# Kernel optimization log

Hardware: AMD Instinct MI355X
Metric: run time of the kernel (lower is better)

## Reference

```python
import jax, jax.numpy as jnp
import numpy as np

B, T, I, H, O, R = 128, 1024, 64, 512, 32, 2
TAU = 0.2
NOISE_STD = 0.05


def setup_inputs() -> dict:
    key = jax.random.key(0)
    ks = jax.random.split(key, 12)
    def xavier(k, shape):
        fan_in, fan_out = shape[1], shape[0]
        lim = float(np.sqrt(6.0 / (fan_in + fan_out)))
        return jax.random.uniform(k, shape, jnp.float32, -lim, lim)
    return {
        "u": jax.random.normal(ks[0], (B, T, I), jnp.float32),
        "x0": jax.random.normal(ks[1], (B, H), jnp.float32),
        "noise": jax.random.normal(ks[2], (T, B, H), jnp.float32),
        "Win_w": xavier(ks[3], (H, I)),
        "Win_b": jnp.zeros((H,), jnp.float32),
        "Wout_w": xavier(ks[4], (O, H)),
        "Wout_b": jax.random.normal(ks[5], (O,), jnp.float32) * 0.01,
        "M_rnn": xavier(ks[6], (H, R)),
        "N_rnn": xavier(ks[7], (H, R)),
        "L_tb": xavier(ks[8], (H, R)),
        "M_tb": xavier(ks[9], (H, R)),
        "N_tb": xavier(ks[10], (H, R)),
    }


def reference(u, x0, noise, Win_w, Win_b, Wout_w, Wout_b,
              M_rnn, N_rnn, L_tb, M_tb, N_tb):
    # mode='cont', form='rate', adv=False
    Hdim = x0.shape[1]
    scale_rnn = 1.0 / Hdim
    scale_tb = 1.0 / (Hdim * Hdim)
    # precompute input projection for all timesteps: [T, B, H]
    inp_t = jnp.transpose(jnp.einsum('bti,hi->bth', u, Win_w) + Win_b, (1, 0, 2))

    def step(x, xs):
        ip, nz = xs                                # [B,H] each
        r = jnp.tanh(x)                            # rate form
        rec_rnn = (r @ N_rnn) @ M_rnn.T * scale_rnn
        rec_tb = ((r @ M_tb) * (r @ N_tb)) @ L_tb.T * scale_tb
        rec_x = rec_rnn + rec_tb + ip
        x_new = x + NOISE_STD * nz + TAU * (-x + rec_x)
        return x_new, x_new

    x_final, traj_t = jax.lax.scan(step, x0, (inp_t, noise))
    traj = jnp.transpose(traj_t, (1, 0, 2))        # [B,T,H]
    output = jnp.tanh(traj) @ Wout_w.T + Wout_b    # [B,T,O]
    return output, x_final, traj
```

## Files before the change

kernel.cpp:

```cpp
#include <hip/hip_runtime.h>

constexpr int kB = 128;
constexpr int kT = 1024;
constexpr int kI = 64;
constexpr int kH = 512;
constexpr int kO = 32;
constexpr float kTau = 0.2f;
constexpr float kNoise = 0.05f;

__device__ __forceinline__ float fast_tanh(float x) {
    float e = __expf(2.0f * x);
    return 1.0f - 2.0f * __builtin_amdgcn_rcpf(e + 1.0f);
}

#define BARW() do { asm volatile("s_waitcnt lgkmcnt(0)" ::: "memory"); \
                    __builtin_amdgcn_s_barrier();                      \
                    asm volatile("" ::: "memory"); } while (0)

template <int CTRL, int RMASK>
__device__ __forceinline__ float dpp_add(float s) {
    return s + __int_as_float(__builtin_amdgcn_update_dpp(
        0, __float_as_int(s), CTRL, RMASK, 0xf, true));
}
__device__ __forceinline__ float wave_sum64_lane63(float s) {
    s = dpp_add<0x111, 0xf>(s);
    s = dpp_add<0x112, 0xf>(s);
    s = dpp_add<0x114, 0xf>(s);
    s = dpp_add<0x118, 0xf>(s);
    s = dpp_add<0x142, 0xa>(s);
    s = dpp_add<0x143, 0xc>(s);
    return s;
}

__global__ __launch_bounds__(512, 2) void scan_kernel(
    const float* __restrict__ u, const float* __restrict__ x0,
    const float* __restrict__ noise, const float* __restrict__ Win_w,
    const float* __restrict__ Win_b, const float* __restrict__ M_rnn,
    const float* __restrict__ N_rnn, const float* __restrict__ L_tb,
    const float* __restrict__ M_tb, const float* __restrict__ N_tb,
    float* __restrict__ traj, float* __restrict__ xfin)
{
    const int b    = blockIdx.x;
    const int h    = threadIdx.x;
    const int wid  = h >> 6;
    const int lane = h & 63;

    __shared__ float red[6 * kH];
    __shared__ __align__(16) float res[8];

    float W[kI];
    #pragma unroll
    for (int i = 0; i < kI; i += 4) {
        float4 w = *(const float4*)&Win_w[h * kI + i];
        W[i] = w.x; W[i + 1] = w.y; W[i + 2] = w.z; W[i + 3] = w.w;
    }
    #pragma unroll
    for (int i = 0; i < kI; ++i) asm volatile("" : "+v"(W[i]));

    const float wb  = Win_b[h];
    const float Nr0 = N_rnn[h * 2], Nr1 = N_rnn[h * 2 + 1];
    const float Mt0 = M_tb[h * 2],  Mt1 = M_tb[h * 2 + 1];
    const float Nt0 = N_tb[h * 2],  Nt1 = N_tb[h * 2 + 1];
    const float sc_rnn = 1.0f / (float)kH;
    const float sc_tb  = 1.0f / ((float)kH * (float)kH);
    const float Mr0 = M_rnn[h * 2] * sc_rnn, Mr1 = M_rnn[h * 2 + 1] * sc_rnn;
    const float Lt0 = L_tb[h * 2] * sc_tb,   Lt1 = L_tb[h * 2 + 1] * sc_tb;

    float x = x0[b * kH + h];

    const float* up  = u + (size_t)b * kT * kI;
    const float* nzp = noise + (size_t)b * kH + h;
    float* tp = traj + (size_t)b * kT * kH + h;

    float4 ur[16];
    {
        const float4* u4 = (const float4*)up;
        #pragma unroll
        for (int i = 0; i < 16; ++i) ur[i] = u4[i];
    }
    float nzA = nzp[0];
    float nzB = nzp[(size_t)kB * kH];

    auto step = [&](int t, float& nzC) {
        float r = fast_tanh(x);
        red[0 * kH + h] = r * Nr0;
        red[1 * kH + h] = r * Nr1;
        red[2 * kH + h] = r * Mt0;
        red[3 * kH + h] = r * Mt1;
        red[4 * kH + h] = r * Nt0;
        red[5 * kH + h] = r * Nt1;
        BARW();
        if (wid < 6) {
            const float* c = red + wid * kH + lane;
            float s0 = c[0]   + c[64];
            float s1 = c[128] + c[192];
            float s2 = c[256] + c[320];
            float s3 = c[384] + c[448];
            float s  = (s0 + s1) + (s2 + s3);
            s = wave_sum64_lane63(s);
            if (lane == 63) res[wid] = s;
        }
        BARW();
        float4 r4 = *(const float4*)&res[0];
        float2 r2 = *(const float2*)&res[4];
        float ip = wb;
        #pragma unroll
        for (int i = 0; i < 16; ++i) {
            ip += ur[i].x * W[4 * i]     + ur[i].y * W[4 * i + 1]
                + ur[i].z * W[4 * i + 2] + ur[i].w * W[4 * i + 3];
        }
        {
            int tn = (t + 1 < kT) ? t + 1 : kT - 1;
            const float4* u4 = (const float4*)(up + (size_t)tn * kI);
            #pragma unroll
            for (int i = 0; i < 16; ++i) ur[i] = u4[i];
        }
        float rec = r4.x * Mr0 + r4.y * Mr1
                  + (r4.z * r2.x) * Lt0 + (r4.w * r2.y) * Lt1 + ip;
        x = (1.0f - kTau) * x + kNoise * nzC + kTau * rec;
        tp[(size_t)t * kH] = x;
        int t2 = (t + 2 < kT) ? t + 2 : kT - 1;
        nzC = nzp[(size_t)t2 * kB * kH];
    };

    for (int t = 0; t < kT; t += 2) {
        step(t, nzA);
        step(t + 1, nzB);
    }
    xfin[b * kH + h] = x;
}

constexpr int R_BLK = 256;
constexpr int H_CHK = 32;
constexpr int AS_LD = 260;

__global__ __launch_bounds__(256, 2) void out_kernel(
    const float* __restrict__ traj, const float* __restrict__ Wout_w,
    const float* __restrict__ Wout_b, float* __restrict__ out)
{
    __shared__ float As[H_CHK][AS_LD];
    __shared__ float Ws[H_CHK][36];

    const int tid = threadIdx.x;
    const size_t row0 = (size_t)blockIdx.x * R_BLK;
    const int og = tid & 3;
    const int rg = tid >> 2;

    float acc[4][8];
    #pragma unroll
    for (int k = 0; k < 4; ++k)
        #pragma unroll
        for (int j = 0; j < 8; ++j) acc[k][j] = 0.f;

    const int lr = tid >> 3;
    const int lc4 = tid & 7;
    const int wo = tid >> 3;
    const int wc = (tid & 7) * 4;

    for (int ch = 0; ch < 16; ++ch) {
        const int hc = ch * H_CHK;
        float4 a[8];
        #pragma unroll
        for (int j = 0; j < 8; ++j) {
            const int r = j * 32 + lr;
            a[j] = *(const float4*)&traj[(row0 + r) * kH + hc + lc4 * 4];
        }
        float4 w = *(const float4*)&Wout_w[wo * kH + hc + wc];
        __syncthreads();
        #pragma unroll
        for (int j = 0; j < 8; ++j) {
            const int r = j * 32 + lr;
            As[lc4 * 4 + 0][r] = fast_tanh(a[j].x);
            As[lc4 * 4 + 1][r] = fast_tanh(a[j].y);
            As[lc4 * 4 + 2][r] = fast_tanh(a[j].z);
            As[lc4 * 4 + 3][r] = fast_tanh(a[j].w);
        }
        Ws[wc + 0][wo] = w.x;
        Ws[wc + 1][wo] = w.y;
        Ws[wc + 2][wo] = w.z;
        Ws[wc + 3][wo] = w.w;
        __syncthreads();
        #pragma unroll
        for (int hh = 0; hh < H_CHK; ++hh) {
            float4 av = *(const float4*)&As[hh][rg * 4];
            float4 w0 = *(const float4*)&Ws[hh][og * 8];
            float4 w1 = *(const float4*)&Ws[hh][og * 8 + 4];
            const float av4[4] = {av.x, av.y, av.z, av.w};
            const float wv[8]  = {w0.x, w0.y, w0.z, w0.w,
                                  w1.x, w1.y, w1.z, w1.w};
            #pragma unroll
            for (int k = 0; k < 4; ++k)
                #pragma unroll
                for (int j = 0; j < 8; ++j)
                    acc[k][j] += av4[k] * wv[j];
        }
    }

    #pragma unroll
    for (int k = 0; k < 4; ++k) {
        const size_t row = row0 + rg * 4 + k;
        float4 v0, v1;
        v0.x = acc[k][0] + Wout_b[og * 8 + 0];
        v0.y = acc[k][1] + Wout_b[og * 8 + 1];
        v0.z = acc[k][2] + Wout_b[og * 8 + 2];
        v0.w = acc[k][3] + Wout_b[og * 8 + 3];
        v1.x = acc[k][4] + Wout_b[og * 8 + 4];
        v1.y = acc[k][5] + Wout_b[og * 8 + 5];
        v1.z = acc[k][6] + Wout_b[og * 8 + 6];
        v1.w = acc[k][7] + Wout_b[og * 8 + 7];
        *(float4*)&out[row * kO + og * 8]     = v0;
        *(float4*)&out[row * kO + og * 8 + 4] = v1;
    }
}

extern "C" void kernel_launch(void* const* d_in, const int* in_sizes, int n_in,
                              void* d_out, int out_size, void* d_ws, size_t ws_size,
                              hipStream_t stream) {
    const float* u      = (const float*)d_in[0];
    const float* x0     = (const float*)d_in[1];
    const float* noise  = (const float*)d_in[2];
    const float* Win_w  = (const float*)d_in[3];
    const float* Win_b  = (const float*)d_in[4];
    const float* Wout_w = (const float*)d_in[5];
    const float* Wout_b = (const float*)d_in[6];
    const float* M_rnn  = (const float*)d_in[7];
    const float* N_rnn  = (const float*)d_in[8];
    const float* L_tb   = (const float*)d_in[9];
    const float* M_tb   = (const float*)d_in[10];
    const float* N_tb   = (const float*)d_in[11];

    float* out  = (float*)d_out;
    float* xfin = out + (size_t)kB * kT * kO;
    float* traj = xfin + (size_t)kB * kH;

    scan_kernel<<<dim3(kB), dim3(kH), 0, stream>>>(
        u, x0, noise, Win_w, Win_b, M_rnn, N_rnn, L_tb, M_tb, N_tb, traj, xfin);
    out_kernel<<<dim3((kB * kT) / R_BLK), dim3(256), 0, stream>>>(
        traj, Wout_w, Wout_b, out);
}
```

Before: 1.466 ms.

## Hoist input projection into separate kernel and shrink scan to one wave per batch

A new parallel kernel computes the input projection plus noise term for all timesteps ahead of time and writes it into the traj buffer. The scan kernel then reads that precomputed term back in place, so it no longer does the 64-wide dot product each step. The scan now runs as a single 64-lane wave per batch row holding 8 hidden units per lane, and it reduces with DPP and readlane, which removes the LDS traffic and both block barriers per step. The out kernel is also rewritten to stage Wout once in LDS and stream traj rows directly, at the cost of an extra full write and read of traj and only 128 single-wave blocks in the serial scan.

Result: slower. 1.728 ms (+17.9%).

```diff
diff --git a/kernel.cpp b/kernel.cpp
--- a/kernel.cpp
+++ b/kernel.cpp
@@ -13,138 +13,171 @@
     return 1.0f - 2.0f * __builtin_amdgcn_rcpf(e + 1.0f);
 }
 
-#define BARW() do { asm volatile("s_waitcnt lgkmcnt(0)" ::: "memory"); \
-                    __builtin_amdgcn_s_barrier();                      \
-                    asm volatile("" ::: "memory"); } while (0)
-
 template <int CTRL, int RMASK>
 __device__ __forceinline__ float dpp_add(float s) {
     return s + __int_as_float(__builtin_amdgcn_update_dpp(
         0, __float_as_int(s), CTRL, RMASK, 0xf, true));
 }
-__device__ __forceinline__ float wave_sum64_lane63(float s) {
-    s = dpp_add<0x111, 0xf>(s);
-    s = dpp_add<0x112, 0xf>(s);
-    s = dpp_add<0x114, 0xf>(s);
-    s = dpp_add<0x118, 0xf>(s);
-    s = dpp_add<0x142, 0xa>(s);
-    s = dpp_add<0x143, 0xc>(s);
-    return s;
-}
-
-__global__ __launch_bounds__(512, 2) void scan_kernel(
-    const float* __restrict__ u, const float* __restrict__ x0,
-    const float* __restrict__ noise, const float* __restrict__ Win_w,
-    const float* __restrict__ Win_b, const float* __restrict__ M_rnn,
+
+constexpr int ROWS_PB = 64;
+
+__global__ __launch_bounds__(512, 2) void inp_kernel(
+    const float* __restrict__ u, const float* __restrict__ Win_w,
+    const float* __restrict__ Win_b, const float* __restrict__ noise,
+    float* __restrict__ traj)
+{
+    const int h = threadIdx.x;
+    const size_t row0 = (size_t)blockIdx.x * ROWS_PB;
+
+    float W[kI];
+    #pragma unroll
+    for (int i = 0; i < kI; i += 4) {
+        float4 w = *(const float4*)&Win_w[(size_t)h * kI + i];
+        W[i] = w.x * kTau; W[i + 1] = w.y * kTau;
+        W[i + 2] = w.z * kTau; W[i + 3] = w.w * kTau;
+    }
+    const float twb = Win_b[h] * kTau;
+
+    for (int r = 0; r < ROWS_PB; ++r) {
+        const size_t row = row0 + r;
+        const int t  = (int)(row & (kT - 1));
+        const int bb = (int)(row >> 10);
+        float nz = noise[((size_t)t * kB + bb) * kH + h];
+        const float* ur = u + row * kI;
+        float ip = twb;
+        #pragma unroll
+        for (int i = 0; i < kI; ++i) ip = fmaf(ur[i], W[i], ip);
+        traj[row * kH + h] = fmaf(kNoise, nz, ip);
+    }
+}
+
+__global__ __launch_bounds__(64) void scan_kernel(
+    const float* __restrict__ x0, const float* __restrict__ M_rnn,
     const float* __restrict__ N_rnn, const float* __restrict__ L_tb,
     const float* __restrict__ M_tb, const float* __restrict__ N_tb,
     float* __restrict__ traj, float* __restrict__ xfin)
 {
     const int b    = blockIdx.x;
-    const int h    = threadIdx.x;
-    const int wid  = h >> 6;
-    const int lane = h & 63;
-
-    __shared__ float red[6 * kH];
-    __shared__ __align__(16) float res[8];
-
-    float W[kI];
-    #pragma unroll
-    for (int i = 0; i < kI; i += 4) {
-        float4 w = *(const float4*)&Win_w[h * kI + i];
-        W[i] = w.x; W[i + 1] = w.y; W[i + 2] = w.z; W[i + 3] = w.w;
-    }
-    #pragma unroll
-    for (int i = 0; i < kI; ++i) asm volatile("" : "+v"(W[i]));
-
-    const float wb  = Win_b[h];
-    const float Nr0 = N_rnn[h * 2], Nr1 = N_rnn[h * 2 + 1];
-    const float Mt0 = M_tb[h * 2],  Mt1 = M_tb[h * 2 + 1];
-    const float Nt0 = N_tb[h * 2],  Nt1 = N_tb[h * 2 + 1];
-    const float sc_rnn = 1.0f / (float)kH;
-    const float sc_tb  = 1.0f / ((float)kH * (float)kH);
-    const float Mr0 = M_rnn[h * 2] * sc_rnn, Mr1 = M_rnn[h * 2 + 1] * sc_rnn;
-    const float Lt0 = L_tb[h * 2] * sc_tb,   Lt1 = L_tb[h * 2 + 1] * sc_tb;
-
-    float x = x0[b * kH + h];
-
-    const float* up  = u + (size_t)b * kT * kI;
-    const float* nzp = noise + (size_t)b * kH + h;
-    float* tp = traj + (size_t)b * kT * kH + h;
-
-    float4 ur[16];
-    {
-        const float4* u4 = (const float4*)up;
-        #pragma unroll
-        for (int i = 0; i < 16; ++i) ur[i] = u4[i];
-    }
-    float nzA = nzp[0];
-    float nzB = nzp[(size_t)kB * kH];
-
-    auto step = [&](int t, float& nzC) {
-        float r = fast_tanh(x);
-        red[0 * kH + h] = r * Nr0;
-        red[1 * kH + h] = r * Nr1;
-        red[2 * kH + h] = r * Mt0;
-        red[3 * kH + h] = r * Mt1;
-        red[4 * kH + h] = r * Nt0;
-        red[5 * kH + h] = r * Nt1;
-        BARW();
-        if (wid < 6) {
-            const float* c = red + wid * kH + lane;
-            float s0 = c[0]   + c[64];
-            float s1 = c[128] + c[192];
-            float s2 = c[256] + c[320];
-            float s3 = c[384] + c[448];
-            float s  = (s0 + s1) + (s2 + s3);
-            s = wave_sum64_lane63(s);
-            if (lane == 63) res[wid] = s;
-        }
-        BARW();
-        float4 r4 = *(const float4*)&res[0];
-        float2 r2 = *(const float2*)&res[4];
-        float ip = wb;
-        #pragma unroll
-        for (int i = 0; i < 16; ++i) {
-            ip += ur[i].x * W[4 * i]     + ur[i].y * W[4 * i + 1]
-                + ur[i].z * W[4 * i + 2] + ur[i].w * W[4 * i + 3];
-        }
-        {
-            int tn = (t + 1 < kT) ? t + 1 : kT - 1;
-            const float4* u4 = (const float4*)(up + (size_t)tn * kI);
-            #pragma unroll
-            for (int i = 0; i < 16; ++i) ur[i] = u4[i];
-        }
-        float rec = r4.x * Mr0 + r4.y * Mr1
-                  + (r4.z * r2.x) * Lt0 + (r4.w * r2.y) * Lt1 + ip;
-        x = (1.0f - kTau) * x + kNoise * nzC + kTau * rec;
-        tp[(size_t)t * kH] = x;
-        int t2 = (t + 2 < kT) ? t + 2 : kT - 1;
-        nzC = nzp[(size_t)t2 * kB * kH];
+    const int lane = threadIdx.x;
+
+    const float sr = kTau / (float)kH;
+    const float st = kTau / ((float)kH * (float)kH);
+
+    float Nr0[8], Nr1[8], Mt0[8], Mt1[8], Nt0[8], Nt1[8];
+    float tMr0[8], tMr1[8], tLt0[8], tLt1[8];
+    float x[8];
+
+    #pragma unroll
+    for (int k = 0; k < 8; ++k) {
+        const int h = lane + 64 * k;
+        float2 v;
+        v = *(const float2*)&N_rnn[2 * h]; Nr0[k] = v.x;      Nr1[k] = v.y;
+        v = *(const float2*)&M_tb[2 * h];  Mt0[k] = v.x;      Mt1[k] = v.y;
+        v = *(const float2*)&N_tb[2 * h];  Nt0[k] = v.x;      Nt1[k] = v.y;
+        v = *(const float2*)&M_rnn[2 * h]; tMr0[k] = v.x * sr; tMr1[k] = v.y * sr;
+        v = *(const float2*)&L_tb[2 * h];  tLt0[k] = v.x * st; tLt1[k] = v.y * st;
+        x[k] = x0[b * kH + h];
+    }
+
+    float* tp = traj + (size_t)b * kT * kH + lane;
+
+    float cA[8], cB[8];
+    #pragma unroll
+    for (int k = 0; k < 8; ++k) {
+        cA[k] = tp[64 * k];
+        cB[k] = tp[kH + 64 * k];
+    }
+
+    auto step = [&](int t, float* c) {
+        float r[8];
+        #pragma unroll
+        for (int k = 0; k < 8; ++k) r[k] = fast_tanh(x[k]);
+
+        float a0 = 0.f, a1 = 0.f, m0 = 0.f, m1 = 0.f, n0 = 0.f, n1 = 0.f;
+        #pragma unroll
+        for (int k = 0; k < 8; ++k) {
+            a0 = fmaf(r[k], Nr0[k], a0);
+            a1 = fmaf(r[k], Nr1[k], a1);
+            m0 = fmaf(r[k], Mt0[k], m0);
+            m1 = fmaf(r[k], Mt1[k], m1);
+            n0 = fmaf(r[k], Nt0[k], n0);
+            n1 = fmaf(r[k], Nt1[k], n1);
+        }
+        #define RSTAGE(CTRL, MASK)                                          \
+            a0 = dpp_add<CTRL, MASK>(a0); a1 = dpp_add<CTRL, MASK>(a1);     \
+            m0 = dpp_add<CTRL, MASK>(m0); m1 = dpp_add<CTRL, MASK>(m1);     \
+            n0 = dpp_add<CTRL, MASK>(n0); n1 = dpp_add<CTRL, MASK>(n1);
+        RSTAGE(0x111, 0xf)
+        RSTAGE(0x112, 0xf)
+        RSTAGE(0x114, 0xf)
+        RSTAGE(0x118, 0xf)
+        RSTAGE(0x142, 0xa)
+        RSTAGE(0x143, 0xc)
+        #undef RSTAGE
+
+        const float sa0 = __int_as_float(
+            __builtin_amdgcn_readlane(__float_as_int(a0), 63));
+        const float sa1 = __int_as_float(
+            __builtin_amdgcn_readlane(__float_as_int(a1), 63));
+        const float sm0 = __int_as_float(
+            __builtin_amdgcn_readlane(__float_as_int(m0), 63));
+        const float sm1 = __int_as_float(
+            __builtin_amdgcn_readlane(__float_as_int(m1), 63));
+        const float sn0 = __int_as_float(
+            __builtin_amdgcn_readlane(__float_as_int(n0), 63));
+        const float sn1 = __int_as_float(
+            __builtin_amdgcn_readlane(__float_as_int(n1), 63));
+        const float p0 = sm0 * sn0;
+        const float p1 = sm1 * sn1;
+
+        #pragma unroll
+        for (int k = 0; k < 8; ++k) {
+            float rc = fmaf(p1, tLt1[k], c[k]);
+            rc = fmaf(p0, tLt0[k], rc);
+            rc = fmaf(sa1, tMr1[k], rc);
+            rc = fmaf(sa0, tMr0[k], rc);
+            x[k] = fmaf(1.0f - kTau, x[k], rc);
+            tp[(size_t)t * kH + 64 * k] = x[k];
+        }
+        const int t2 = (t + 2) & (kT - 1);
+        #pragma unroll
+        for (int k = 0; k < 8; ++k)
+            c[k] = tp[(size_t)t2 * kH + 64 * k];
     };
 
     for (int t = 0; t < kT; t += 2) {
-        step(t, nzA);
-        step(t + 1, nzB);
-    }
-    xfin[b * kH + h] = x;
-}
-
-constexpr int R_BLK = 256;
-constexpr int H_CHK = 32;
-constexpr int AS_LD = 260;
-
-__global__ __launch_bounds__(256, 2) void out_kernel(
+        step(t,     cA);
+        step(t + 1, cB);
+    }
+    #pragma unroll
+    for (int k = 0; k < 8; ++k)
+        xfin[b * kH + lane + 64 * k] = x[k];
+}
+
+__global__ __launch_bounds__(256) void out_kernel(
     const float* __restrict__ traj, const float* __restrict__ Wout_w,
     const float* __restrict__ Wout_b, float* __restrict__ out)
 {
-    __shared__ float As[H_CHK][AS_LD];
-    __shared__ float Ws[H_CHK][36];
-
+    __shared__ float Wl[kH][kO];
     const int tid = threadIdx.x;
-    const size_t row0 = (size_t)blockIdx.x * R_BLK;
+    {
+        const int o  = tid >> 3;
+        const int cb = (tid & 7) * 64;
+        #pragma unroll
+        for (int j = 0; j < 64; j += 4) {
+            float4 w = *(const float4*)&Wout_w[(size_t)o * kH + cb + j];
+            Wl[cb + j + 0][o] = w.x;
+            Wl[cb + j + 1][o] = w.y;
+            Wl[cb + j + 2][o] = w.z;
+            Wl[cb + j + 3][o] = w.w;
+        }
+    }
+    __syncthreads();
+
     const int og = tid & 3;
     const int rg = tid >> 2;
+    const size_t row0 = (size_t)blockIdx.x * 256 + (size_t)rg * 4;
+    const float* tb = traj + row0 * kH;
 
     float acc[4][8];
     #pragma unroll
@@ -152,53 +185,44 @@
         #pragma unroll
         for (int j = 0; j < 8; ++j) acc[k][j] = 0.f;
 
-    const int lr = tid >> 3;
-    const int lc4 = tid & 7;
-    const int wo = tid >> 3;
-    const int wc = (tid & 7) * 4;
-
-    for (int ch = 0; ch < 16; ++ch) {
-        const int hc = ch * H_CHK;
-        float4 a[8];
-        #pragma unroll
-        for (int j = 0; j < 8; ++j) {
-            const int r = j * 32 + lr;
-            a[j] = *(const float4*)&traj[(row0 + r) * kH + hc + lc4 * 4];
-        }
-        float4 w = *(const float4*)&Wout_w[wo * kH + hc + wc];
-        __syncthreads();
-        #pragma unroll
-        for (int j = 0; j < 8; ++j) {
-            const int r = j * 32 + lr;
-            As[lc4 * 4 + 0][r] = fast_tanh(a[j].x);
-            As[lc4 * 4 + 1][r] = fast_tanh(a[j].y);
-            As[lc4 * 4 + 2][r] = fast_tanh(a[j].z);
-            As[lc4 * 4 + 3][r] = fast_tanh(a[j].w);
-        }
-        Ws[wc + 0][wo] = w.x;
-        Ws[wc + 1][wo] = w.y;
-        Ws[wc + 2][wo] = w.z;
-        Ws[wc + 3][wo] = w.w;
-        __syncthreads();
-        #pragma unroll
-        for (int hh = 0; hh < H_CHK; ++hh) {
-            float4 av = *(const float4*)&As[hh][rg * 4];
-            float4 w0 = *(const float4*)&Ws[hh][og * 8];
-            float4 w1 = *(const float4*)&Ws[hh][og * 8 + 4];
-            const float av4[4] = {av.x, av.y, av.z, av.w};
-            const float wv[8]  = {w0.x, w0.y, w0.z, w0.w,
-                                  w1.x, w1.y, w1.z, w1.w};
+    float4 a[4], n[4];
+    #pragma unroll
+    for (int k = 0; k < 4; ++k) a[k] = *(const float4*)&tb[k * kH];
+
+    for (int hh = 0; hh < kH; hh += 4) {
+        const int hn = hh + 4;
+        if (hn < kH) {
+            #pragma unroll
+            for (int k = 0; k < 4; ++k)
+                n[k] = *(const float4*)&tb[k * kH + hn];
+        }
+        float tv[4][4];
+        #pragma unroll
+        for (int k = 0; k < 4; ++k) {
+            tv[k][0] = fast_tanh(a[k].x);
+            tv[k][1] = fast_tanh(a[k].y);
+            tv[k][2] = fast_tanh(a[k].z);
+            tv[k][3] = fast_tanh(a[k].w);
+        }
+        #pragma unroll
+        for (int j = 0; j < 4; ++j) {
+            float4 w0 = *(const float4*)&Wl[hh + j][og * 8];
+            float4 w1 = *(const float4*)&Wl[hh + j][og * 8 + 4];
+            const float wv[8] = {w0.x, w0.y, w0.z, w0.w,
+                                 w1.x, w1.y, w1.z, w1.w};
             #pragma unroll
             for (int k = 0; k < 4; ++k)
                 #pragma unroll
-                for (int j = 0; j < 8; ++j)
-                    acc[k][j] += av4[k] * wv[j];
-        }
+                for (int jj = 0; jj < 8; ++jj)
+                    acc[k][jj] = fmaf(tv[k][j], wv[jj], acc[k][jj]);
+        }
+        #pragma unroll
+        for (int k = 0; k < 4; ++k) a[k] = n[k];
     }
 
     #pragma unroll
     for (int k = 0; k < 4; ++k) {
-        const size_t row = row0 + rg * 4 + k;
+        const size_t row = row0 + k;
         float4 v0, v1;
         v0.x = acc[k][0] + Wout_b[og * 8 + 0];
         v0.y = acc[k][1] + Wout_b[og * 8 + 1];
@@ -233,8 +257,10 @@
     float* xfin = out + (size_t)kB * kT * kO;
     float* traj = xfin + (size_t)kB * kH;
 
-    scan_kernel<<<dim3(kB), dim3(kH), 0, stream>>>(
-        u, x0, noise, Win_w, Win_b, M_rnn, N_rnn, L_tb, M_tb, N_tb, traj, xfin);
-    out_kernel<<<dim3((kB * kT) / R_BLK), dim3(256), 0, stream>>>(
+    inp_kernel<<<dim3((kB * kT) / ROWS_PB), dim3(512), 0, stream>>>(
+        u, Win_w, Win_b, noise, traj);
+    scan_kernel<<<dim3(kB), dim3(64), 0, stream>>>(
+        x0, M_rnn, N_rnn, L_tb, M_tb, N_tb, traj, xfin);
+    out_kernel<<<dim3((kB * kT) / 256), dim3(256), 0, stream>>>(
         traj, Wout_w, Wout_b, out);
 }
```
